# Performance work log

Measured on AMD Instinct MI355X. Metric: run time of the kernel, lower is better.

Reference implementation:

```python
import jax, jax.numpy as jnp
import numpy as np


def setup_inputs() -> dict:
    key = jax.random.key(0)
    k1, k2, k3 = jax.random.split(key, 3)
    B, IN, OUT = 8192, 2048, 2048
    x = jax.random.normal(k1, (B, IN), dtype=jnp.float32)
    # kaiming_uniform_(a=sqrt(5)) on [OUT, IN] -> bound = sqrt(6/((1+5)*IN)) = 1/sqrt(IN)
    wb = 1.0 / np.sqrt(IN)
    weight = jax.random.uniform(k2, (OUT, IN), dtype=jnp.float32, minval=-wb, maxval=wb)
    bb = 1.0 / np.sqrt(IN)
    bias = jax.random.uniform(k3, (OUT,), dtype=jnp.float32, minval=-bb, maxval=bb)
    return {"x": x, "weight": weight, "bias": bias}


def reference(x, weight, bias):
    # out[b,o] = sum_i (x[b,i] + w[o,i]) = rowsum(x)[b] + rowsum(w)[o]
    # (identical math to the O(B*O*I) broadcast-sum, computed in O(B*I + O*I + B*O))
    x_sum = jnp.sum(x, axis=1)        # [B]
    w_sum = jnp.sum(weight, axis=1)   # [O]
    out = x_sum[:, None] + w_sum[None, :]  # [B, O]
    out = out * bias                  # note: original does `output *= self.bias`
    return out
```

## Files before the change

kernel.cpp:

```cpp
#include <hip/hip_runtime.h>


#define B_DIM 8192
#define IN_DIM 2048
#define OUT_DIM 2048

__global__ __launch_bounds__(256) void rowsum_kernel(const float* __restrict__ x,
                                                     const float* __restrict__ w,
                                                     const float* __restrict__ bias,
                                                     float* __restrict__ xsum,
                                                     float* __restrict__ wsb) {
    const int row = blockIdx.x;
    const int tid = threadIdx.x;
    const bool is_w = row >= B_DIM;
    const float* src = is_w ? (w + (size_t)(row - B_DIM) * IN_DIM)
                            : (x + (size_t)row * IN_DIM);
    const float4* src4 = reinterpret_cast<const float4*>(src);
    float4 a = src4[tid];
    float4 b = src4[tid + 256];
    float s = (a.x + a.y) + (a.z + a.w) + (b.x + b.y) + (b.z + b.w);

    #pragma unroll
    for (int off = 32; off > 0; off >>= 1)
        s += __shfl_down(s, off, 64);

    __shared__ float ls[4];
    if ((tid & 63) == 0) ls[tid >> 6] = s;
    __syncthreads();
    if (tid == 0) {
        float tot = (ls[0] + ls[1]) + (ls[2] + ls[3]);
        if (is_w) {
            int o = row - B_DIM;
            wsb[o] = tot * bias[o];
        } else {
            xsum[row] = tot;
        }
    }
}

__global__ __launch_bounds__(256) void write_kernel(const float* __restrict__ xsum,
                                                    const float* __restrict__ wsb,
                                                    const float* __restrict__ bias,
                                                    float4* __restrict__ out4) {
    const float4* bias4 = reinterpret_cast<const float4*>(bias);
    const float4* wsb4  = reinterpret_cast<const float4*>(wsb);
    const int total4 = B_DIM * (OUT_DIM / 4);
    int idx = blockIdx.x * blockDim.x + threadIdx.x;
    const int stride = gridDim.x * blockDim.x;
    for (; idx < total4; idx += stride) {
        const int b  = idx >> 9;
        const int oc = idx & 511;
        const float  xs = xsum[b];
        const float4 bi = bias4[oc];
        const float4 ws = wsb4[oc];
        float4 o;
        o.x = fmaf(xs, bi.x, ws.x);
        o.y = fmaf(xs, bi.y, ws.y);
        o.z = fmaf(xs, bi.z, ws.z);
        o.w = fmaf(xs, bi.w, ws.w);
        out4[idx] = o;
    }
}

extern "C" void kernel_launch(void* const* d_in, const int* in_sizes, int n_in,
                              void* d_out, int out_size, void* d_ws, size_t ws_size,
                              hipStream_t stream) {
    const float* x    = (const float*)d_in[0];
    const float* w    = (const float*)d_in[1];
    const float* bias = (const float*)d_in[2];
    float* out  = (float*)d_out;
    float* xsum = (float*)d_ws;
    float* wsb  = xsum + B_DIM;

    rowsum_kernel<<<B_DIM + OUT_DIM, 256, 0, stream>>>(x, w, bias, xsum, wsb);
    write_kernel<<<2048, 256, 0, stream>>>(xsum, wsb, bias, (float4*)out);
}
```

Measured before the change: 30.33 us.

## Fuse x row reduction with output row write in one kernel

Splits the weight rowsum into its own small kernel and fuses the x rowsum with the output broadcast write, so each block reduces one x row and then writes the matching output row. This removes the xsum workspace round trip and lets reads of x overlap with output writes within a single kernel. Each block now also reloads bias and wsb rows, and the weight reduction runs as its own serialized phase.

```diff
diff --git a/kernel.cpp b/kernel.cpp
--- a/kernel.cpp
+++ b/kernel.cpp
@@ -5,61 +5,71 @@
 #define IN_DIM 2048
 #define OUT_DIM 2048
 
-__global__ __launch_bounds__(256) void rowsum_kernel(const float* __restrict__ x,
-                                                     const float* __restrict__ w,
-                                                     const float* __restrict__ bias,
-                                                     float* __restrict__ xsum,
-                                                     float* __restrict__ wsb) {
-    const int row = blockIdx.x;
-    const int tid = threadIdx.x;
-    const bool is_w = row >= B_DIM;
-    const float* src = is_w ? (w + (size_t)(row - B_DIM) * IN_DIM)
-                            : (x + (size_t)row * IN_DIM);
-    const float4* src4 = reinterpret_cast<const float4*>(src);
-    float4 a = src4[tid];
-    float4 b = src4[tid + 256];
-    float s = (a.x + a.y) + (a.z + a.w) + (b.x + b.y) + (b.z + b.w);
+__device__ __forceinline__ float sum8(float4 a, float4 b) {
+    return ((a.x + a.y) + (a.z + a.w)) + ((b.x + b.y) + (b.z + b.w));
+}
 
+__device__ __forceinline__ float wave_reduce(float s) {
     #pragma unroll
     for (int off = 32; off > 0; off >>= 1)
         s += __shfl_down(s, off, 64);
+    return s;
+}
+
+__global__ __launch_bounds__(256) void wsb_kernel(const float* __restrict__ w,
+                                                  const float* __restrict__ bias,
+                                                  float* __restrict__ wsb) {
+    const int row = blockIdx.x;
+    const int tid = threadIdx.x;
+    const float4* src4 = reinterpret_cast<const float4*>(w + (size_t)row * IN_DIM);
+    float4 a = src4[tid];
+    float4 b = src4[tid + 256];
+    float s = wave_reduce(sum8(a, b));
 
     __shared__ float ls[4];
     if ((tid & 63) == 0) ls[tid >> 6] = s;
     __syncthreads();
-    if (tid == 0) {
-        float tot = (ls[0] + ls[1]) + (ls[2] + ls[3]);
-        if (is_w) {
-            int o = row - B_DIM;
-            wsb[o] = tot * bias[o];
-        } else {
-            xsum[row] = tot;
-        }
-    }
+    if (tid == 0)
+        wsb[row] = ((ls[0] + ls[1]) + (ls[2] + ls[3])) * bias[row];
 }
 
-__global__ __launch_bounds__(256) void write_kernel(const float* __restrict__ xsum,
-                                                    const float* __restrict__ wsb,
-                                                    const float* __restrict__ bias,
-                                                    float4* __restrict__ out4) {
+__global__ __launch_bounds__(256) void fused_row_kernel(const float* __restrict__ x,
+                                                        const float* __restrict__ bias,
+                                                        const float* __restrict__ wsb,
+                                                        float4* __restrict__ out4) {
+    const int row = blockIdx.x;
+    const int tid = threadIdx.x;
+    const float4* src4 = reinterpret_cast<const float4*>(x + (size_t)row * IN_DIM);
     const float4* bias4 = reinterpret_cast<const float4*>(bias);
     const float4* wsb4  = reinterpret_cast<const float4*>(wsb);
-    const int total4 = B_DIM * (OUT_DIM / 4);
-    int idx = blockIdx.x * blockDim.x + threadIdx.x;
-    const int stride = gridDim.x * blockDim.x;
-    for (; idx < total4; idx += stride) {
-        const int b  = idx >> 9;
-        const int oc = idx & 511;
-        const float  xs = xsum[b];
-        const float4 bi = bias4[oc];
-        const float4 ws = wsb4[oc];
-        float4 o;
-        o.x = fmaf(xs, bi.x, ws.x);
-        o.y = fmaf(xs, bi.y, ws.y);
-        o.z = fmaf(xs, bi.z, ws.z);
-        o.w = fmaf(xs, bi.w, ws.w);
-        out4[idx] = o;
-    }
+
+    float4 a   = src4[tid];
+    float4 b   = src4[tid + 256];
+    float4 bi0 = bias4[tid];
+    float4 bi1 = bias4[tid + 256];
+    float4 ws0 = wsb4[tid];
+    float4 ws1 = wsb4[tid + 256];
+
+    float s = wave_reduce(sum8(a, b));
+
+    __shared__ float ls[4];
+    if ((tid & 63) == 0) ls[tid >> 6] = s;
+    __syncthreads();
+    const float xs = (ls[0] + ls[1]) + (ls[2] + ls[3]);
+
+    float4 o0, o1;
+    o0.x = fmaf(xs, bi0.x, ws0.x);
+    o0.y = fmaf(xs, bi0.y, ws0.y);
+    o0.z = fmaf(xs, bi0.z, ws0.z);
+    o0.w = fmaf(xs, bi0.w, ws0.w);
+    o1.x = fmaf(xs, bi1.x, ws1.x);
+    o1.y = fmaf(xs, bi1.y, ws1.y);
+    o1.z = fmaf(xs, bi1.z, ws1.z);
+    o1.w = fmaf(xs, bi1.w, ws1.w);
+
+    const size_t base = (size_t)row * (OUT_DIM / 4);
+    out4[base + tid]       = o0;
+    out4[base + tid + 256] = o1;
 }
 
 extern "C" void kernel_launch(void* const* d_in, const int* in_sizes, int n_in,
@@ -68,10 +78,9 @@
     const float* x    = (const float*)d_in[0];
     const float* w    = (const float*)d_in[1];
     const float* bias = (const float*)d_in[2];
-    float* out  = (float*)d_out;
-    float* xsum = (float*)d_ws;
-    float* wsb  = xsum + B_DIM;
+    float* out = (float*)d_out;
+    float* wsb = (float*)d_ws;
 
-    rowsum_kernel<<<B_DIM + OUT_DIM, 256, 0, stream>>>(x, w, bias, xsum, wsb);
-    write_kernel<<<2048, 256, 0, stream>>>(xsum, wsb, bias, (float4*)out);
+    wsb_kernel<<<OUT_DIM, 256, 0, stream>>>(w, bias, wsb);
+    fused_row_kernel<<<B_DIM, 256, 0, stream>>>(x, bias, wsb, (float4*)out);
 }
```

Result: faster. 29.68 us (-2.1%).

## Fuse x row-sum with output write; wave-per-row reductions with nontemporal access

Applied to the files above, without the earlier changes.

Splits the work into a small kernel that reduces weight rows and scales them by bias, and a fused kernel where each wavefront reduces one x row and immediately writes that output row. This removes the xsum round trip through global memory and the shared-memory block reduction, replacing the latter with a wave-level xor butterfly. Loads of x/w and stores of out use nontemporal hints to limit cache pollution. The block count for the main kernel is now fixed by B, and each wave re-reads bias and wsb from cache.

```diff
diff --git a/kernel.cpp b/kernel.cpp
--- a/kernel.cpp
+++ b/kernel.cpp
@@ -5,60 +5,69 @@
 #define IN_DIM 2048
 #define OUT_DIM 2048
 
-__global__ __launch_bounds__(256) void rowsum_kernel(const float* __restrict__ x,
-                                                     const float* __restrict__ w,
-                                                     const float* __restrict__ bias,
-                                                     float* __restrict__ xsum,
-                                                     float* __restrict__ wsb) {
-    const int row = blockIdx.x;
-    const int tid = threadIdx.x;
-    const bool is_w = row >= B_DIM;
-    const float* src = is_w ? (w + (size_t)(row - B_DIM) * IN_DIM)
-                            : (x + (size_t)row * IN_DIM);
-    const float4* src4 = reinterpret_cast<const float4*>(src);
-    float4 a = src4[tid];
-    float4 b = src4[tid + 256];
-    float s = (a.x + a.y) + (a.z + a.w) + (b.x + b.y) + (b.z + b.w);
+typedef float f32x4 __attribute__((ext_vector_type(4)));
 
+__device__ __forceinline__ float butterfly_reduce(float s) {
     #pragma unroll
-    for (int off = 32; off > 0; off >>= 1)
-        s += __shfl_down(s, off, 64);
-
-    __shared__ float ls[4];
-    if ((tid & 63) == 0) ls[tid >> 6] = s;
-    __syncthreads();
-    if (tid == 0) {
-        float tot = (ls[0] + ls[1]) + (ls[2] + ls[3]);
-        if (is_w) {
-            int o = row - B_DIM;
-            wsb[o] = tot * bias[o];
-        } else {
-            xsum[row] = tot;
-        }
-    }
+    for (int off = 32; off; off >>= 1)
+        s += __shfl_xor(s, off, 64);
+    return s;
 }
 
-__global__ __launch_bounds__(256) void write_kernel(const float* __restrict__ xsum,
-                                                    const float* __restrict__ wsb,
-                                                    const float* __restrict__ bias,
-                                                    float4* __restrict__ out4) {
-    const float4* bias4 = reinterpret_cast<const float4*>(bias);
-    const float4* wsb4  = reinterpret_cast<const float4*>(wsb);
-    const int total4 = B_DIM * (OUT_DIM / 4);
-    int idx = blockIdx.x * blockDim.x + threadIdx.x;
-    const int stride = gridDim.x * blockDim.x;
-    for (; idx < total4; idx += stride) {
-        const int b  = idx >> 9;
-        const int oc = idx & 511;
-        const float  xs = xsum[b];
-        const float4 bi = bias4[oc];
-        const float4 ws = wsb4[oc];
-        float4 o;
+__global__ __launch_bounds__(256) void wsb_kernel(const float* __restrict__ w,
+                                                  const float* __restrict__ bias,
+                                                  float* __restrict__ wsb) {
+    const int wave = threadIdx.x >> 6;
+    const int lane = threadIdx.x & 63;
+    const int row  = (blockIdx.x << 2) + wave;
+    const f32x4* src4 = reinterpret_cast<const f32x4*>(w + (size_t)row * IN_DIM);
+
+    f32x4 v[8];
+    #pragma unroll
+    for (int k = 0; k < 8; ++k)
+        v[k] = __builtin_nontemporal_load(&src4[lane + (k << 6)]);
+    float s = 0.f;
+    #pragma unroll
+    for (int k = 0; k < 8; ++k)
+        s += (v[k].x + v[k].y) + (v[k].z + v[k].w);
+    s = butterfly_reduce(s);
+    if (lane == 0)
+        wsb[row] = s * bias[row];
+}
+
+__global__ __launch_bounds__(256) void fused_row_kernel(const float* __restrict__ x,
+                                                        const float* __restrict__ bias,
+                                                        const float* __restrict__ wsb,
+                                                        f32x4* __restrict__ out4) {
+    const int wave = threadIdx.x >> 6;
+    const int lane = threadIdx.x & 63;
+    const int row  = (blockIdx.x << 2) + wave;
+    const f32x4* src4  = reinterpret_cast<const f32x4*>(x + (size_t)row * IN_DIM);
+    const f32x4* bias4 = reinterpret_cast<const f32x4*>(bias);
+    const f32x4* wsb4  = reinterpret_cast<const f32x4*>(wsb);
+
+    f32x4 v[8];
+    #pragma unroll
+    for (int k = 0; k < 8; ++k)
+        v[k] = __builtin_nontemporal_load(&src4[lane + (k << 6)]);
+    float s = 0.f;
+    #pragma unroll
+    for (int k = 0; k < 8; ++k)
+        s += (v[k].x + v[k].y) + (v[k].z + v[k].w);
+    const float xs = butterfly_reduce(s);
+
+    f32x4* orow = out4 + (size_t)row * (OUT_DIM / 4);
+    #pragma unroll
+    for (int k = 0; k < 8; ++k) {
+        const int i = lane + (k << 6);
+        const f32x4 bi = bias4[i];
+        const f32x4 ws = wsb4[i];
+        f32x4 o;
         o.x = fmaf(xs, bi.x, ws.x);
         o.y = fmaf(xs, bi.y, ws.y);
         o.z = fmaf(xs, bi.z, ws.z);
         o.w = fmaf(xs, bi.w, ws.w);
-        out4[idx] = o;
+        __builtin_nontemporal_store(o, &orow[i]);
     }
 }
 
@@ -68,10 +77,9 @@
     const float* x    = (const float*)d_in[0];
     const float* w    = (const float*)d_in[1];
     const float* bias = (const float*)d_in[2];
-    float* out  = (float*)d_out;
-    float* xsum = (float*)d_ws;
-    float* wsb  = xsum + B_DIM;
+    float* out = (float*)d_out;
+    float* wsb = (float*)d_ws;
 
-    rowsum_kernel<<<B_DIM + OUT_DIM, 256, 0, stream>>>(x, w, bias, xsum, wsb);
-    write_kernel<<<2048, 256, 0, stream>>>(xsum, wsb, bias, (float4*)out);
+    wsb_kernel<<<OUT_DIM / 4, 256, 0, stream>>>(w, bias, wsb);
+    fused_row_kernel<<<B_DIM / 4, 256, 0, stream>>>(x, bias, wsb, (f32x4*)out);
 }
```

Measured after the change: 32.99 us. 8.8% more time.
